# Kernel optimization log

Hardware: AMD Instinct MI355X
Metric: run time of the kernel (lower is better)

The kernel has to match this reference:

```python
import jax, jax.numpy as jnp
import numpy as np

B, T, D, H = 4, 3072, 1024, 16
HD = D // H

def setup_inputs() -> dict:
    key = jax.random.key(0)
    ks = jax.random.split(key, 7)
    s = 1.0 / np.sqrt(D)
    x = jax.random.normal(ks[0], (B, T, D), dtype=jnp.float32)
    Wq = jax.random.normal(ks[1], (D, D), dtype=jnp.float32) * s
    Wk = jax.random.normal(ks[2], (D, D), dtype=jnp.float32) * s
    Wv = jax.random.normal(ks[3], (D, D), dtype=jnp.float32) * s
    Wo = jax.random.normal(ks[4], (D, D), dtype=jnp.float32) * s
    bo = jnp.zeros((D,), dtype=jnp.float32)
    Wconv = jax.random.normal(ks[5], (D, D, 3), dtype=jnp.float32) * (1.0 / np.sqrt(3 * D))  # (out, in, kw)
    return {"x": x, "Wq": Wq, "Wk": Wk, "Wv": Wv, "Wo": Wo, "bo": bo, "Wconv": Wconv}

def reference(x, Wq, Wk, Wv, Wo, bo, Wconv):
    b, t, d = x.shape
    # stride-3 conv pooling of K/V stream (Conv1d(D, D, 3, stride=3, bias=False))
    kc = jax.lax.conv_general_dilated(
        x.transpose(0, 2, 1), Wconv, window_strides=(3,), padding='VALID',
        dimension_numbers=('NCH', 'OIH', 'NCH')).transpose(0, 2, 1)  # (B, T//3, D)
    k_tmp = jnp.concatenate([x[:, :1, :], kc], axis=1)  # (B, Tk, D)
    tk = k_tmp.shape[1]
    # comparison-based bias mask: masked where 3*k_idx >= q_idx + 0.001
    q_idx = jnp.arange(t, dtype=jnp.float32)
    k_idx = jnp.arange(tk, dtype=jnp.float32)
    mask = (k_idx[None, :] * 3.0 >= q_idx[:, None] + 0.001).astype(x.dtype)  # (T, Tk)
    # projections (torch Linear: y = x @ W.T)
    q = x @ Wq.T
    k = k_tmp @ Wk.T
    v = k_tmp @ Wv.T
    q = q.reshape(b, t, H, HD).transpose(0, 2, 1, 3)   # (B, H, T, HD)
    k = k.reshape(b, tk, H, HD).transpose(0, 2, 1, 3)  # (B, H, Tk, HD)
    v = v.reshape(b, tk, H, HD).transpose(0, 2, 1, 3)
    scores = jnp.einsum('bhqd,bhkd->bhqk', q, k) * (HD ** -0.5)
    scores = scores + mask * jnp.asarray(-1e9, dtype=x.dtype)
    p = jax.nn.softmax(scores, axis=-1)  # dropout is identity in eval (p=0)
    o = jnp.einsum('bhqk,bhkd->bhqd', p, v)
    o = o.transpose(0, 2, 1, 3).reshape(b, t, d)
    return o @ Wo.T + bo
```

## Files before the change

### kernel.cpp

```cpp
#include <hip/hip_runtime.h>
#include <hip/hip_bf16.h>
#include <cstdint>
#include <cstddef>

typedef __attribute__((ext_vector_type(8))) __bf16 bf16x8;
typedef __attribute__((ext_vector_type(4))) __bf16 bf16x4;
typedef __attribute__((ext_vector_type(4))) float  floatx4;

#define MFMA16x16x32(a, b, c) __builtin_amdgcn_mfma_f32_16x16x32_bf16((a), (b), (c), 0, 0, 0)

#define ATTN_SC 0.18033688011112042f

__device__ __forceinline__ void gload_lds16(const void* g, void* l) {
  __builtin_amdgcn_global_load_lds((const __attribute__((address_space(1))) void*)g,
                                   (__attribute__((address_space(3))) void*)l,
                                   16, 0, 0);
}


__global__ void prep_kernel(const float* __restrict__ x,
                            const float* __restrict__ Wq, const float* __restrict__ Wk,
                            const float* __restrict__ Wv, const float* __restrict__ Wo,
                            const float* __restrict__ Wconv,
                            __bf16* __restrict__ xb,
                            __bf16* __restrict__ wqb, __bf16* __restrict__ wkb,
                            __bf16* __restrict__ wvb, __bf16* __restrict__ wob,
                            __bf16* __restrict__ wc2, __bf16* __restrict__ ktmp) {
  const int bid = blockIdx.x, tid = threadIdx.x;
  if (bid < 4096) {
    const int which = bid >> 10;
    const float* src = (which == 0) ? Wq : (which == 1) ? Wk : (which == 2) ? Wv : Wo;
    __bf16* dst = (which == 0) ? wqb : (which == 1) ? wkb : (which == 2) ? wvb : wob;
    const int i = (bid & 1023) * 256 + tid;
    floatx4 v = *(const floatx4*)(src + (size_t)i * 4);
    bf16x4 o; o[0] = (__bf16)v[0]; o[1] = (__bf16)v[1]; o[2] = (__bf16)v[2]; o[3] = (__bf16)v[3];
    *(bf16x4*)(dst + (size_t)i * 4) = o;
  } else if (bid < 5120) {
    const int t = (bid - 4096) * 256 + tid;
    const int o = t >> 8, c = t & 255;
    const float* base = Wconv + (size_t)o * 3072 + c * 12;
    float f[12];
    *(floatx4*)(f)     = *(const floatx4*)(base);
    *(floatx4*)(f + 4) = *(const floatx4*)(base + 4);
    *(floatx4*)(f + 8) = *(const floatx4*)(base + 8);
#pragma unroll
    for (int kw = 0; kw < 3; ++kw) {
      bf16x4 q;
#pragma unroll
      for (int j = 0; j < 4; ++j) q[j] = (__bf16)f[3 * j + kw];
      *(bf16x4*)(wc2 + (size_t)o * 3072 + kw * 1024 + c * 4) = q;
    }
  } else if (bid < 5136) {
    const int i = (bid - 5120) * 256 + tid;
    const int b = i >> 10, c = i & 1023;
    ktmp[(size_t)b * 1025 * 1024 + c] = (__bf16)x[(size_t)b * 3072 * 1024 + c];
  } else {
    const int i = (bid - 5136) * 256 + tid;
    floatx4 v = *(const floatx4*)(x + (size_t)i * 4);
    bf16x4 o; o[0] = (__bf16)v[0]; o[1] = (__bf16)v[1]; o[2] = (__bf16)v[2]; o[3] = (__bf16)v[3];
    *(bf16x4*)(xb + (size_t)i * 4) = o;
  }
}

__global__ void vtrans_kernel(const __bf16* __restrict__ V, __bf16* __restrict__ Vt) {
  __shared__ __attribute__((aligned(16))) __bf16 tile[64][72];
  const int tid = threadIdx.x;
  const int bh = blockIdx.y;
  const int b = bh >> 4, h = bh & 15;
  const int t0 = blockIdx.x * 64;
  const int r = tid >> 3, s = tid & 7;
#pragma unroll
  for (int p = 0; p < 2; ++p) {
    const int t = p * 32 + r;
    bf16x8 v = *(const bf16x8*)(V + ((size_t)(b * 1025 + t0 + t)) * 1024 + h * 64 + s * 8);
    *(bf16x8*)(&tile[t][s * 8]) = v;
  }
  __syncthreads();
#pragma unroll
  for (int p = 0; p < 2; ++p) {
    const int d = p * 32 + r;
    bf16x8 o;
#pragma unroll
    for (int e = 0; e < 8; ++e) o[e] = tile[s * 8 + e][d];
    *(bf16x8*)(Vt + ((size_t)bh * 64 + d) * 1024 + t0 + s * 8) = o;
  }
}


template <int MODE>
__device__ __forceinline__ void gemm_body(
    const __bf16* __restrict__ A, const __bf16* __restrict__ Bw, void* __restrict__ Cout,
    const float* __restrict__ bias, int N, int K, int m0, int n0,
    __bf16* As, __bf16* Bs)
{
  const int tid  = threadIdx.x;
  const int wave = tid >> 6;
  const int lane = tid & 63;
  const int g    = lane >> 4;
  const int ln   = lane & 15;
  const int wr = (wave >> 1) * 64;
  const int wc = (wave & 1) * 64;
  const int lr = lane >> 2;
  const int lc = (lane & 3) * 8;

  floatx4 acc[4][4];
#pragma unroll
  for (int i = 0; i < 4; ++i)
#pragma unroll
    for (int j = 0; j < 4; ++j) { floatx4 z = {0.f, 0.f, 0.f, 0.f}; acc[i][j] = z; }

  for (int k0 = 0; k0 < K; k0 += 32) {
    __syncthreads();
#pragma unroll
    for (int i = 0; i < 2; ++i) {
      const int rr = (wave * 2 + i) * 16 + lr;
      gload_lds16(A  + (size_t)(m0 + rr) * K + k0 + lc, As + rr * 32 + lc);
      gload_lds16(Bw + (size_t)(n0 + rr) * K + k0 + lc, Bs + rr * 32 + lc);
    }
    __syncthreads();
    bf16x8 af[4], bfr[4];
#pragma unroll
    for (int i = 0; i < 4; ++i) af[i]  = *(const bf16x8*)(As + (wr + i * 16 + ln) * 32 + g * 8);
#pragma unroll
    for (int j = 0; j < 4; ++j) bfr[j] = *(const bf16x8*)(Bs + (wc + j * 16 + ln) * 32 + g * 8);
#pragma unroll
    for (int i = 0; i < 4; ++i)
#pragma unroll
      for (int j = 0; j < 4; ++j)
        acc[i][j] = MFMA16x16x32(af[i], bfr[j], acc[i][j]);
  }

#pragma unroll
  for (int j = 0; j < 4; ++j) {
    const int col = n0 + wc + j * 16 + ln;
    float bj = 0.f;
    if (MODE == 2) bj = bias[col];
#pragma unroll
    for (int i = 0; i < 4; ++i)
#pragma unroll
      for (int r = 0; r < 4; ++r) {
        const int row = m0 + wr + i * 16 + g * 4 + r;
        if (MODE == 2) {
          ((float*)Cout)[(size_t)row * N + col] = acc[i][j][r] + bj;
        } else if (MODE == 1) {
          const size_t orow = (size_t)(row >> 10) * 1025 + 1 + (row & 1023);
          ((__bf16*)Cout)[orow * 1024 + col] = (__bf16)acc[i][j][r];
        } else if (MODE == 4) {
          ((__bf16*)Cout)[(size_t)row * N + col] = (__bf16)(acc[i][j][r] * ATTN_SC);
        } else {
          ((__bf16*)Cout)[(size_t)row * N + col] = (__bf16)acc[i][j][r];
        }
      }
  }
}

__global__ __launch_bounds__(256) void gemm_convq_kernel(
    const __bf16* __restrict__ xb, const __bf16* __restrict__ wc2,
    const __bf16* __restrict__ wqb, __bf16* __restrict__ ktmp, __bf16* __restrict__ qb)
{
  __shared__ __attribute__((aligned(16))) __bf16 As[128 * 32];
  __shared__ __attribute__((aligned(16))) __bf16 Bs[128 * 32];
  const int bid = blockIdx.x;
  if (bid < 256) {
    gemm_body<1>(xb, wc2, ktmp, nullptr, 1024, 3072, (bid >> 3) * 128, (bid & 7) * 128, As, Bs);
  } else {
    const int t = bid - 256;
    gemm_body<4>(xb, wqb, qb, nullptr, 1024, 1024, (t >> 3) * 128, (t & 7) * 128, As, Bs);
  }
}

__global__ __launch_bounds__(256) void gemm_kv_kernel(
    const __bf16* __restrict__ ktmp, const __bf16* __restrict__ wkb,
    const __bf16* __restrict__ wvb, __bf16* __restrict__ kb, __bf16* __restrict__ vb)
{
  __shared__ __attribute__((aligned(16))) __bf16 As[128 * 32];
  __shared__ __attribute__((aligned(16))) __bf16 Bs[128 * 32];
  const __bf16* Bw = blockIdx.z ? wvb : wkb;
  __bf16* C = blockIdx.z ? vb : kb;
  gemm_body<0>(ktmp, Bw, C, nullptr, 1024, 1024, blockIdx.y * 128, blockIdx.x * 128, As, Bs);
}

__global__ __launch_bounds__(256) void gemm_o_kernel(
    const __bf16* __restrict__ ob, const __bf16* __restrict__ wob,
    float* __restrict__ out, const float* __restrict__ bo)
{
  __shared__ __attribute__((aligned(16))) __bf16 As[128 * 32];
  __shared__ __attribute__((aligned(16))) __bf16 Bs[128 * 32];
  gemm_body<2>(ob, wob, out, bo, 1024, 1024, blockIdx.y * 128, blockIdx.x * 128, As, Bs);
}


__global__ __launch_bounds__(256) void attn_kernel(
    const __bf16* __restrict__ Q, const __bf16* __restrict__ Kk,
    const __bf16* __restrict__ Vt, __bf16* __restrict__ O)
{
  __shared__ __attribute__((aligned(16))) __bf16 Kd[2][64 * 64];
  __shared__ __attribute__((aligned(16))) __bf16 Vd[2][64 * 64];
  __shared__ __attribute__((aligned(16))) __bf16 Ps[4][32 * 64];

  const int tid  = threadIdx.x;
  const int wave = tid >> 6;
  const int lane = tid & 63;
  const int g    = lane >> 4;
  const int ln   = lane & 15;

  const int l    = blockIdx.x;
  const int xcd  = l & 7;
  const int b    = xcd >> 1;
  const int rest = l >> 3;
  const int h    = rest & 15;
  const int qt   = ((11 - (rest >> 4)) << 1) | (xcd & 1);
  const int q0   = qt * 128 + wave * 32;

  const size_t qrow0 = (size_t)b * 3072 + q0;
  const size_t krow0 = (size_t)b * 1025;
  const size_t vtrow = ((size_t)(b * 16 + h)) * 64;
  const int hc = h * 64;
  const int sw = (ln & 7) << 3;
  __bf16* Pw = Ps[wave];

  const int srow = lane >> 3;
  const int scol = (lane & 7) * 8;

  auto stage = [&](int kt, int bb) {
    const int kb0 = kt * 64;
#pragma unroll
    for (int i = 0; i < 2; ++i) {
      const int rr = (wave * 2 + i) * 8 + srow;
      gload_lds16(Kk + (krow0 + kb0 + rr) * 1024 + hc + scol,
                  Kd[bb] + (size_t)rr * 64 + scol);
      gload_lds16(Vt + (vtrow + rr) * 1024 + kb0 + scol,
                  Vd[bb] + (size_t)rr * 64 + scol);
    }
  };

  bf16x8 qf[2][2];
#pragma unroll
  for (int i = 0; i < 2; ++i)
#pragma unroll
    for (int kc = 0; kc < 2; ++kc)
      qf[i][kc] = *(const bf16x8*)(Q + (qrow0 + i * 16 + ln) * 1024 + hc + kc * 32 + g * 8);

  floatx4 oacc[2][4];
  floatx4 oal[2];
#pragma unroll
  for (int i = 0; i < 2; ++i) {
    floatx4 z = {0.f, 0.f, 0.f, 0.f};
    oal[i] = z;
#pragma unroll
    for (int dt = 0; dt < 4; ++dt) oacc[i][dt] = z;
  }

  bf16x8 ones;
#pragma unroll
  for (int e = 0; e < 8; ++e) ones[e] = (__bf16)1.0f;

  const int nkt_blk = (((qt * 128 + 127) / 3) >> 6) + 1;
  const int nfull   = (q0 >= 189) ? ((q0 - 189) / 192 + 1) : 0;

  stage(0, 0);

  for (int kt = 0; kt < nkt_blk; ++kt) {
    const int bb = kt & 1;
    __syncthreads();
    if (kt + 1 < nkt_blk) stage(kt + 1, bb ^ 1);
    const int kb0 = kt * 64;
    const bool masked = (kt >= nfull);

    bf16x8 kf[4][2];
#pragma unroll
    for (int jk = 0; jk < 4; ++jk)
#pragma unroll
      for (int kc = 0; kc < 2; ++kc)
        kf[jk][kc] = *(const bf16x8*)(Kd[bb] + (jk * 16 + ln) * 64 + kc * 32 + g * 8);

#pragma unroll
    for (int jk = 0; jk < 4; ++jk)
#pragma unroll
      for (int i = 0; i < 2; ++i) {
        floatx4 s = {0.f, 0.f, 0.f, 0.f};
        s = MFMA16x16x32(kf[jk][0], qf[i][0], s);
        s = MFMA16x16x32(kf[jk][1], qf[i][1], s);
        float p[4];
#pragma unroll
        for (int r = 0; r < 4; ++r) {
          float e = __builtin_amdgcn_exp2f(s[r]);
          if (masked) {
            const int key = kb0 + jk * 16 + 4 * g + r;
            const int q   = q0 + i * 16 + ln;
            e = (3 * key <= q) ? e : 0.f;
          }
          p[r] = e;
        }
        bf16x4 pk;
        pk[0] = (__bf16)p[0]; pk[1] = (__bf16)p[1]; pk[2] = (__bf16)p[2]; pk[3] = (__bf16)p[3];
        *(bf16x4*)(Pw + (i * 16 + ln) * 64 + ((jk * 16 + 4 * g) ^ sw)) = pk;
      }

#pragma unroll
    for (int kc = 0; kc < 2; ++kc) {
      bf16x8 pf0 = *(const bf16x8*)(Pw + (ln) * 64      + ((kc * 32 + g * 8) ^ sw));
      bf16x8 pf1 = *(const bf16x8*)(Pw + (16 + ln) * 64 + ((kc * 32 + g * 8) ^ sw));
      oal[0] = MFMA16x16x32(ones, pf0, oal[0]);
      oal[1] = MFMA16x16x32(ones, pf1, oal[1]);
#pragma unroll
      for (int dt = 0; dt < 4; ++dt) {
        bf16x8 vf = *(const bf16x8*)(Vd[bb] + (dt * 16 + ln) * 64 + kc * 32 + g * 8);
        oacc[0][dt] = MFMA16x16x32(vf, pf0, oacc[0][dt]);
        oacc[1][dt] = MFMA16x16x32(vf, pf1, oacc[1][dt]);
      }
    }
  }

#pragma unroll
  for (int i = 0; i < 2; ++i) {
    const float inv = 1.0f / oal[i][0];
    const size_t row = qrow0 + i * 16 + ln;
#pragma unroll
    for (int dt = 0; dt < 4; ++dt) {
      bf16x4 o4;
#pragma unroll
      for (int r = 0; r < 4; ++r) o4[r] = (__bf16)(oacc[i][dt][r] * inv);
      *(bf16x4*)(O + row * 1024 + hc + dt * 16 + 4 * g) = o4;
    }
  }
}


extern "C" void kernel_launch(void* const* d_in, const int* in_sizes, int n_in,
                              void* d_out, int out_size, void* d_ws, size_t ws_size,
                              hipStream_t stream) {
  (void)in_sizes; (void)n_in; (void)out_size; (void)ws_size;
  const float* x     = (const float*)d_in[0];
  const float* Wq    = (const float*)d_in[1];
  const float* Wk    = (const float*)d_in[2];
  const float* Wv    = (const float*)d_in[3];
  const float* Wo    = (const float*)d_in[4];
  const float* bo    = (const float*)d_in[5];
  const float* Wconv = (const float*)d_in[6];

  char* ws = (char*)d_ws;
  const size_t SZ_XQ = (size_t)12288 * 1024 * 2;
  const size_t SZ_KT = (size_t)4224 * 1024 * 2;
  const size_t SZ_W  = (size_t)1024 * 1024 * 2;

  __bf16* xb   = (__bf16*)(ws);
  __bf16* qb   = (__bf16*)(ws + SZ_XQ);
  __bf16* ktmp = (__bf16*)(ws + 2 * SZ_XQ);
  __bf16* kb   = (__bf16*)(ws + 2 * SZ_XQ + SZ_KT);
  __bf16* vb   = (__bf16*)(ws + 2 * SZ_XQ + 2 * SZ_KT);
  __bf16* wqb  = (__bf16*)(ws + 2 * SZ_XQ + 3 * SZ_KT);
  __bf16* wkb  = (__bf16*)(ws + 2 * SZ_XQ + 3 * SZ_KT + SZ_W);
  __bf16* wvb  = (__bf16*)(ws + 2 * SZ_XQ + 3 * SZ_KT + 2 * SZ_W);
  __bf16* wob  = (__bf16*)(ws + 2 * SZ_XQ + 3 * SZ_KT + 3 * SZ_W);
  __bf16* wc2  = (__bf16*)(ws + 2 * SZ_XQ + 3 * SZ_KT + 4 * SZ_W);
  __bf16* vt   = xb;

  prep_kernel<<<dim3(17424), dim3(256), 0, stream>>>(x, Wq, Wk, Wv, Wo, Wconv,
                                                     xb, wqb, wkb, wvb, wob, wc2, ktmp);
  gemm_convq_kernel<<<dim3(1024), dim3(256), 0, stream>>>(xb, wc2, wqb, ktmp, qb);
  gemm_kv_kernel<<<dim3(8, 33, 2), dim3(256), 0, stream>>>(ktmp, wkb, wvb, kb, vb);
  vtrans_kernel<<<dim3(16, 64), dim3(256), 0, stream>>>(vb, vt);
  attn_kernel<<<dim3(1536), dim3(256), 0, stream>>>(qb, kb, vt, qb);
  gemm_o_kernel<<<dim3(8, 96, 1), dim3(256), 0, stream>>>(qb, wob, (float*)d_out, bo);
}
```

Measured before the change: 333.3 us.

## Rewrite GEMMs with 128x256 tiles, 4-stage LDS pipeline, swizzle, XCD-aware mapping

Measured after the change: 377.7 us. +13.3%, slower.

```diff
diff --git a/kernel.cpp b/kernel.cpp
--- a/kernel.cpp
+++ b/kernel.cpp
@@ -88,7 +88,7 @@
 
 
 template <int MODE>
-__device__ __forceinline__ void gemm_body(
+__device__ __forceinline__ void gemm8_body(
     const __bf16* __restrict__ A, const __bf16* __restrict__ Bw, void* __restrict__ Cout,
     const float* __restrict__ bias, int N, int K, int m0, int n0,
     __bf16* As, __bf16* Bs)
@@ -98,10 +98,31 @@
   const int lane = tid & 63;
   const int g    = lane >> 4;
   const int ln   = lane & 15;
-  const int wr = (wave >> 1) * 64;
-  const int wc = (wave & 1) * 64;
-  const int lr = lane >> 2;
-  const int lc = (lane & 3) * 8;
+  const int wr   = (wave >> 2) * 64;
+  const int wc   = (wave & 3) * 64;
+
+  const int prow = tid >> 3;
+  const int pc   = tid & 7;
+  const int ca   = pc ^ (prow & 7);
+  const size_t aSrc  = (size_t)(m0 + prow + ((ca >> 2) << 6)) * K + ((ca & 3) << 3);
+  const size_t bSrc0 = (size_t)(n0 + prow + ((ca >> 2) << 7)) * K + ((ca & 3) << 3);
+  const size_t bSrc1 = bSrc0 + (size_t)64 * K;
+
+  int aOff[4], bOff[4];
+#pragma unroll
+  for (int i = 0; i < 4; ++i) {
+    const int ra = wr + i * 16 + ln;
+    const int pr = ra & 63;
+    const int c  = ((ra >> 6) << 2) + g;
+    aOff[i] = pr * 64 + ((c ^ (pr & 7)) << 3);
+  }
+#pragma unroll
+  for (int j = 0; j < 4; ++j) {
+    const int rb = wc + j * 16 + ln;
+    const int pr = rb & 127;
+    const int c  = ((rb >> 7) << 2) + g;
+    bOff[j] = pr * 64 + ((c ^ (pr & 7)) << 3);
+  }
 
   floatx4 acc[4][4];
 #pragma unroll
@@ -109,26 +130,52 @@
 #pragma unroll
     for (int j = 0; j < 4; ++j) { floatx4 z = {0.f, 0.f, 0.f, 0.f}; acc[i][j] = z; }
 
-  for (int k0 = 0; k0 < K; k0 += 32) {
-    __syncthreads();
-#pragma unroll
-    for (int i = 0; i < 2; ++i) {
-      const int rr = (wave * 2 + i) * 16 + lr;
-      gload_lds16(A  + (size_t)(m0 + rr) * K + k0 + lc, As + rr * 32 + lc);
-      gload_lds16(Bw + (size_t)(n0 + rr) * K + k0 + lc, Bs + rr * 32 + lc);
-    }
-    __syncthreads();
-    bf16x8 af[4], bfr[4];
-#pragma unroll
-    for (int i = 0; i < 4; ++i) af[i]  = *(const bf16x8*)(As + (wr + i * 16 + ln) * 32 + g * 8);
-#pragma unroll
-    for (int j = 0; j < 4; ++j) bfr[j] = *(const bf16x8*)(Bs + (wc + j * 16 + ln) * 32 + g * 8);
+  __bf16* const ad0 = As + (tid << 3);
+  __bf16* const bd0 = Bs + (tid << 3);
+
+  auto STAGE = [&](int t, int half) {
+    const int koff = t * 64 + ((half & 1) << 5);
+    gload_lds16(A  + aSrc  + koff, ad0 + (half << 12));
+    gload_lds16(Bw + bSrc0 + koff, bd0 + (half << 13));
+    gload_lds16(Bw + bSrc1 + koff, bd0 + (half << 13) + 4096);
+  };
+
+  auto COMPUTE = [&](int half) {
+    __builtin_amdgcn_sched_barrier(0);
+    const __bf16* ah = As + (half << 12);
+    const __bf16* bh = Bs + (half << 13);
+    bf16x8 af[4], bf[4];
+#pragma unroll
+    for (int i = 0; i < 4; ++i) af[i] = *(const bf16x8*)(ah + aOff[i]);
+#pragma unroll
+    for (int j = 0; j < 4; ++j) bf[j] = *(const bf16x8*)(bh + bOff[j]);
+    asm volatile("s_waitcnt lgkmcnt(0)" ::: "memory");
+    __builtin_amdgcn_sched_barrier(0);
+    __builtin_amdgcn_s_setprio(1);
 #pragma unroll
     for (int i = 0; i < 4; ++i)
 #pragma unroll
       for (int j = 0; j < 4; ++j)
-        acc[i][j] = MFMA16x16x32(af[i], bfr[j], acc[i][j]);
-  }
+        acc[i][j] = MFMA16x16x32(af[i], bf[j], acc[i][j]);
+    __builtin_amdgcn_s_setprio(0);
+  };
+
+  STAGE(0, 0);
+  STAGE(0, 1);
+  const int HT = K >> 5;
+  for (int h = 0; h < HT - 2; ++h) {
+    STAGE((h + 2) >> 1, (h + 2) & 3);
+    asm volatile("s_waitcnt vmcnt(6)" ::: "memory");
+    __builtin_amdgcn_s_barrier();
+    COMPUTE(h & 3);
+    __builtin_amdgcn_s_barrier();
+  }
+  asm volatile("s_waitcnt vmcnt(3)" ::: "memory");
+  __builtin_amdgcn_s_barrier();
+  COMPUTE((HT - 2) & 3);
+  asm volatile("s_waitcnt vmcnt(0)" ::: "memory");
+  __builtin_amdgcn_s_barrier();
+  COMPUTE((HT - 1) & 3);
 
 #pragma unroll
   for (int j = 0; j < 4; ++j) {
@@ -154,39 +201,43 @@
   }
 }
 
-__global__ __launch_bounds__(256) void gemm_convq_kernel(
+__global__ __launch_bounds__(512, 2) void gemm_convq_kernel(
     const __bf16* __restrict__ xb, const __bf16* __restrict__ wc2,
     const __bf16* __restrict__ wqb, __bf16* __restrict__ ktmp, __bf16* __restrict__ qb)
 {
-  __shared__ __attribute__((aligned(16))) __bf16 As[128 * 32];
-  __shared__ __attribute__((aligned(16))) __bf16 Bs[128 * 32];
-  const int bid = blockIdx.x;
-  if (bid < 256) {
-    gemm_body<1>(xb, wc2, ktmp, nullptr, 1024, 3072, (bid >> 3) * 128, (bid & 7) * 128, As, Bs);
+  __shared__ __attribute__((aligned(16))) __bf16 As[16384];
+  __shared__ __attribute__((aligned(16))) __bf16 Bs[32768];
+  const int xcd = blockIdx.x & 7, s = blockIdx.x >> 3;
+  if (s < 16) {
+    const int id = xcd * 16 + s;
+    gemm8_body<1>(xb, wc2, ktmp, nullptr, 1024, 3072, (id >> 2) * 128, (id & 3) * 256, As, Bs);
   } else {
-    const int t = bid - 256;
-    gemm_body<4>(xb, wqb, qb, nullptr, 1024, 1024, (t >> 3) * 128, (t & 7) * 128, As, Bs);
-  }
-}
-
-__global__ __launch_bounds__(256) void gemm_kv_kernel(
+    const int id = xcd * 48 + (s - 16);
+    gemm8_body<4>(xb, wqb, qb, nullptr, 1024, 1024, (id >> 2) * 128, (id & 3) * 256, As, Bs);
+  }
+}
+
+__global__ __launch_bounds__(512, 2) void gemm_kv_kernel(
     const __bf16* __restrict__ ktmp, const __bf16* __restrict__ wkb,
     const __bf16* __restrict__ wvb, __bf16* __restrict__ kb, __bf16* __restrict__ vb)
 {
-  __shared__ __attribute__((aligned(16))) __bf16 As[128 * 32];
-  __shared__ __attribute__((aligned(16))) __bf16 Bs[128 * 32];
-  const __bf16* Bw = blockIdx.z ? wvb : wkb;
-  __bf16* C = blockIdx.z ? vb : kb;
-  gemm_body<0>(ktmp, Bw, C, nullptr, 1024, 1024, blockIdx.y * 128, blockIdx.x * 128, As, Bs);
-}
-
-__global__ __launch_bounds__(256) void gemm_o_kernel(
+  __shared__ __attribute__((aligned(16))) __bf16 As[16384];
+  __shared__ __attribute__((aligned(16))) __bf16 Bs[32768];
+  const int id = (blockIdx.x & 7) * 33 + (blockIdx.x >> 3);
+  const int p  = (id >= 132) ? 1 : 0;
+  const int rest = id - p * 132;
+  gemm8_body<0>(ktmp, p ? wvb : wkb, p ? vb : kb, nullptr, 1024, 1024,
+                (rest >> 2) * 128, (rest & 3) * 256, As, Bs);
+}
+
+__global__ __launch_bounds__(512, 2) void gemm_o_kernel(
     const __bf16* __restrict__ ob, const __bf16* __restrict__ wob,
     float* __restrict__ out, const float* __restrict__ bo)
 {
-  __shared__ __attribute__((aligned(16))) __bf16 As[128 * 32];
-  __shared__ __attribute__((aligned(16))) __bf16 Bs[128 * 32];
-  gemm_body<2>(ob, wob, out, bo, 1024, 1024, blockIdx.y * 128, blockIdx.x * 128, As, Bs);
+  __shared__ __attribute__((aligned(16))) __bf16 As[16384];
+  __shared__ __attribute__((aligned(16))) __bf16 Bs[32768];
+  const int id = (blockIdx.x & 7) * 48 + (blockIdx.x >> 3);
+  gemm8_body<2>(ob, wob, out, bo, 1024, 1024, (id >> 2) * 128, (id & 3) * 256, As, Bs);
 }
 
 
@@ -358,9 +409,9 @@
 
   prep_kernel<<<dim3(17424), dim3(256), 0, stream>>>(x, Wq, Wk, Wv, Wo, Wconv,
                                                      xb, wqb, wkb, wvb, wob, wc2, ktmp);
-  gemm_convq_kernel<<<dim3(1024), dim3(256), 0, stream>>>(xb, wc2, wqb, ktmp, qb);
-  gemm_kv_kernel<<<dim3(8, 33, 2), dim3(256), 0, stream>>>(ktmp, wkb, wvb, kb, vb);
+  gemm_convq_kernel<<<dim3(512), dim3(512), 0, stream>>>(xb, wc2, wqb, ktmp, qb);
+  gemm_kv_kernel<<<dim3(264), dim3(512), 0, stream>>>(ktmp, wkb, wvb, kb, vb);
   vtrans_kernel<<<dim3(16, 64), dim3(256), 0, stream>>>(vb, vt);
   attn_kernel<<<dim3(1536), dim3(256), 0, stream>>>(qb, kb, vt, qb);
-  gemm_o_kernel<<<dim3(8, 96, 1), dim3(256), 0, stream>>>(qb, wob, (float*)d_out, bo);
-}
+  gemm_o_kernel<<<dim3(384), dim3(512), 0, stream>>>(qb, wob, (float*)d_out, bo);
+}
```

## Replace GEMMs with 256x256 double-buffered swizzled tiles and split-K conv with work queue

Applied to the files above, without the earlier changes.

Result: slower. 359.4 us (+7.8%).

```diff
diff --git a/kernel.cpp b/kernel.cpp
--- a/kernel.cpp
+++ b/kernel.cpp
@@ -5,6 +5,7 @@
 
 typedef __attribute__((ext_vector_type(8))) __bf16 bf16x8;
 typedef __attribute__((ext_vector_type(4))) __bf16 bf16x4;
+typedef __attribute__((ext_vector_type(8))) _Float16 halfx8;
 typedef __attribute__((ext_vector_type(4))) float  floatx4;
 
 #define MFMA16x16x32(a, b, c) __builtin_amdgcn_mfma_f32_16x16x32_bf16((a), (b), (c), 0, 0, 0)
@@ -25,8 +26,10 @@
                             __bf16* __restrict__ xb,
                             __bf16* __restrict__ wqb, __bf16* __restrict__ wkb,
                             __bf16* __restrict__ wvb, __bf16* __restrict__ wob,
-                            __bf16* __restrict__ wc2, __bf16* __restrict__ ktmp) {
+                            __bf16* __restrict__ wc2, __bf16* __restrict__ ktmp,
+                            unsigned* __restrict__ cnt) {
   const int bid = blockIdx.x, tid = threadIdx.x;
+  if (bid == 0 && tid == 0) *cnt = 0;
   if (bid < 4096) {
     const int which = bid >> 10;
     const float* src = (which == 0) ? Wq : (which == 1) ? Wk : (which == 2) ? Wv : Wo;
@@ -88,9 +91,9 @@
 
 
 template <int MODE>
-__device__ __forceinline__ void gemm_body(
+__device__ __forceinline__ void gemm256_body(
     const __bf16* __restrict__ A, const __bf16* __restrict__ Bw, void* __restrict__ Cout,
-    const float* __restrict__ bias, int N, int K, int m0, int n0,
+    const float* __restrict__ bias, int lda, int ldb, int m0, int n0, int mMax,
     __bf16* As, __bf16* Bs)
 {
   const int tid  = threadIdx.x;
@@ -98,37 +101,98 @@
   const int lane = tid & 63;
   const int g    = lane >> 4;
   const int ln   = lane & 15;
-  const int wr = (wave >> 1) * 64;
-  const int wc = (wave & 1) * 64;
-  const int lr = lane >> 2;
-  const int lc = (lane & 3) * 8;
-
-  floatx4 acc[4][4];
-#pragma unroll
-  for (int i = 0; i < 4; ++i)
+  const int wr   = (wave >> 2) * 128;
+  const int wc   = (wave & 3) * 64;
+
+  const int prow = tid >> 3;
+  const int ca   = (tid & 7) ^ (prow & 7);
+  const size_t aS = (size_t)(m0 + prow) * lda + ca * 8;
+  const size_t bS = (size_t)(n0 + prow) * ldb + ca * 8;
+  const size_t a64 = (size_t)64 * lda, b64 = (size_t)64 * ldb;
+
+  const int sx0 = ((g ^ (ln & 7)) << 3);
+  const int sx1 = (((4 + g) ^ (ln & 7)) << 3);
+
+  floatx4 acc[8][4];
+#pragma unroll
+  for (int i = 0; i < 8; ++i)
 #pragma unroll
     for (int j = 0; j < 4; ++j) { floatx4 z = {0.f, 0.f, 0.f, 0.f}; acc[i][j] = z; }
 
-  for (int k0 = 0; k0 < K; k0 += 32) {
-    __syncthreads();
-#pragma unroll
-    for (int i = 0; i < 2; ++i) {
-      const int rr = (wave * 2 + i) * 16 + lr;
-      gload_lds16(A  + (size_t)(m0 + rr) * K + k0 + lc, As + rr * 32 + lc);
-      gload_lds16(Bw + (size_t)(n0 + rr) * K + k0 + lc, Bs + rr * 32 + lc);
-    }
-    __syncthreads();
-    bf16x8 af[4], bfr[4];
-#pragma unroll
-    for (int i = 0; i < 4; ++i) af[i]  = *(const bf16x8*)(As + (wr + i * 16 + ln) * 32 + g * 8);
-#pragma unroll
-    for (int j = 0; j < 4; ++j) bfr[j] = *(const bf16x8*)(Bs + (wc + j * 16 + ln) * 32 + g * 8);
-#pragma unroll
-    for (int i = 0; i < 4; ++i)
-#pragma unroll
-      for (int j = 0; j < 4; ++j)
-        acc[i][j] = MFMA16x16x32(af[i], bfr[j], acc[i][j]);
-  }
+  auto STG_A = [&](int t, int buf, int a) {
+    gload_lds16(A + aS + a * a64 + (size_t)t * 64, As + (buf << 14) + (a << 12) + (tid << 3));
+  };
+  auto STG_B = [&](int t, int buf, int a) {
+    gload_lds16(Bw + bS + a * b64 + (size_t)t * 64, Bs + (buf << 14) + (a << 12) + (tid << 3));
+  };
+
+  bf16x8 bfr[4][2];
+  bf16x8 aE[2][2], aO[2][2];
+
+#define RD_B(Bb)                                                                   \
+  { _Pragma("unroll")                                                              \
+    for (int j_ = 0; j_ < 4; ++j_) {                                               \
+      bfr[j_][0] = *(const bf16x8*)((Bb) + (wc + 16 * j_ + ln) * 64 + sx0);        \
+      bfr[j_][1] = *(const bf16x8*)((Bb) + (wc + 16 * j_ + ln) * 64 + sx1);        \
+    } }
+
+#define RD_A(SET, Ab, q)                                                           \
+  { _Pragma("unroll")                                                              \
+    for (int i_ = 0; i_ < 2; ++i_) {                                               \
+      SET[i_][0] = *(const bf16x8*)((Ab) + (wr + 16 * (2 * (q) + i_) + ln) * 64 + sx0); \
+      SET[i_][1] = *(const bf16x8*)((Ab) + (wr + 16 * (2 * (q) + i_) + ln) * 64 + sx1); \
+    } }
+
+#define MF_Q(SET, q)                                                               \
+  { __builtin_amdgcn_s_setprio(1);                                                 \
+    _Pragma("unroll")                                                              \
+    for (int c_ = 0; c_ < 2; ++c_)                                                 \
+      _Pragma("unroll")                                                            \
+      for (int i_ = 0; i_ < 2; ++i_)                                               \
+        _Pragma("unroll")                                                          \
+        for (int j_ = 0; j_ < 4; ++j_)                                             \
+          acc[2 * (q) + i_][j_] = MFMA16x16x32(SET[i_][c_], bfr[j_][c_], acc[2 * (q) + i_][j_]); \
+    __builtin_amdgcn_s_setprio(0); }
+
+  const int NT = 16;
+
+  STG_A(0, 0, 0); STG_A(0, 0, 1); STG_A(0, 0, 2); STG_A(0, 0, 3);
+  STG_B(0, 0, 0); STG_B(0, 0, 1); STG_B(0, 0, 2); STG_B(0, 0, 3);
+  asm volatile("s_waitcnt vmcnt(0)" ::: "memory");
+  __builtin_amdgcn_s_barrier();
+  __builtin_amdgcn_sched_barrier(0);
+  RD_A(aE, As, 0);
+
+  for (int t = 0; t < NT; ++t) {
+    const int buf = t & 1;
+    const __bf16* Ab  = As + (buf << 14);
+    const __bf16* Bb  = Bs + (buf << 14);
+    const __bf16* Abn = As + ((buf ^ 1) << 14);
+    const bool more = (t + 1 < NT);
+    if (more) { STG_A(t + 1, buf ^ 1, 0); STG_A(t + 1, buf ^ 1, 1); STG_B(t + 1, buf ^ 1, 0); }
+    RD_B(Bb);
+    RD_A(aO, Ab, 1);
+    MF_Q(aE, 0);
+    if (more) { STG_A(t + 1, buf ^ 1, 2); STG_A(t + 1, buf ^ 1, 3); STG_B(t + 1, buf ^ 1, 1); }
+    RD_A(aE, Ab, 2);
+    MF_Q(aO, 1);
+    if (more) { STG_B(t + 1, buf ^ 1, 2); STG_B(t + 1, buf ^ 1, 3); }
+    RD_A(aO, Ab, 3);
+    MF_Q(aE, 2);
+    if (more) {
+      asm volatile("s_waitcnt vmcnt(0)" ::: "memory");
+      __builtin_amdgcn_s_barrier();
+      __builtin_amdgcn_sched_barrier(0);
+      RD_A(aE, Abn, 0);
+    }
+    MF_Q(aO, 3);
+    __builtin_amdgcn_s_barrier();
+    __builtin_amdgcn_sched_barrier(0);
+  }
+
+#undef RD_B
+#undef RD_A
+#undef MF_Q
 
 #pragma unroll
   for (int j = 0; j < 4; ++j) {
@@ -136,57 +200,94 @@
     float bj = 0.f;
     if (MODE == 2) bj = bias[col];
 #pragma unroll
-    for (int i = 0; i < 4; ++i)
+    for (int i = 0; i < 8; ++i)
 #pragma unroll
       for (int r = 0; r < 4; ++r) {
         const int row = m0 + wr + i * 16 + g * 4 + r;
         if (MODE == 2) {
-          ((float*)Cout)[(size_t)row * N + col] = acc[i][j][r] + bj;
+          ((float*)Cout)[(size_t)row * 1024 + col] = acc[i][j][r] + bj;
         } else if (MODE == 1) {
           const size_t orow = (size_t)(row >> 10) * 1025 + 1 + (row & 1023);
           ((__bf16*)Cout)[orow * 1024 + col] = (__bf16)acc[i][j][r];
         } else if (MODE == 4) {
-          ((__bf16*)Cout)[(size_t)row * N + col] = (__bf16)(acc[i][j][r] * ATTN_SC);
+          ((__bf16*)Cout)[(size_t)row * 1024 + col] = (__bf16)(acc[i][j][r] * ATTN_SC);
+        } else if (MODE == 5) {
+          ((_Float16*)Cout)[(size_t)row * 1024 + col] = (_Float16)acc[i][j][r];
         } else {
-          ((__bf16*)Cout)[(size_t)row * N + col] = (__bf16)acc[i][j][r];
+          if (row < mMax) ((__bf16*)Cout)[(size_t)row * 1024 + col] = (__bf16)acc[i][j][r];
         }
       }
   }
 }
 
-__global__ __launch_bounds__(256) void gemm_convq_kernel(
+__global__ __launch_bounds__(512, 2) void gemm_convq_kernel(
     const __bf16* __restrict__ xb, const __bf16* __restrict__ wc2,
-    const __bf16* __restrict__ wqb, __bf16* __restrict__ ktmp, __bf16* __restrict__ qb)
+    const __bf16* __restrict__ wqb, __bf16* __restrict__ ktmp, __bf16* __restrict__ qb,
+    _Float16* __restrict__ P0, _Float16* __restrict__ P1, unsigned* __restrict__ cnt)
 {
-  __shared__ __attribute__((aligned(16))) __bf16 As[128 * 32];
-  __shared__ __attribute__((aligned(16))) __bf16 Bs[128 * 32];
-  const int bid = blockIdx.x;
-  if (bid < 256) {
-    gemm_body<1>(xb, wc2, ktmp, nullptr, 1024, 3072, (bid >> 3) * 128, (bid & 7) * 128, As, Bs);
-  } else {
-    const int t = bid - 256;
-    gemm_body<4>(xb, wqb, qb, nullptr, 1024, 1024, (t >> 3) * 128, (t & 7) * 128, As, Bs);
-  }
-}
-
-__global__ __launch_bounds__(256) void gemm_kv_kernel(
+  __shared__ __attribute__((aligned(16))) __bf16 As[32768];
+  __shared__ __attribute__((aligned(16))) __bf16 Bs[32768];
+  __shared__ unsigned widx;
+  for (;;) {
+    if (threadIdx.x == 0) widx = atomicAdd(cnt, 1u);
+    __syncthreads();
+    const unsigned it = widx;
+    __syncthreads();
+    if (it >= 384u) break;
+    if (it < 192u) {
+      const int tap = (int)it >> 6, tile = (int)it & 63;
+      const int m0 = (tile >> 2) * 256, n0 = (tile & 3) * 256;
+      if (tap == 2)
+        gemm256_body<1>(xb + 2048, wc2 + 2048, ktmp, nullptr, 3072, 3072, m0, n0, 1 << 30, As, Bs);
+      else if (tap == 1)
+        gemm256_body<5>(xb + 1024, wc2 + 1024, P1, nullptr, 3072, 3072, m0, n0, 1 << 30, As, Bs);
+      else
+        gemm256_body<5>(xb, wc2, P0, nullptr, 3072, 3072, m0, n0, 1 << 30, As, Bs);
+    } else {
+      const int qid = (int)it - 192;
+      gemm256_body<4>(xb, wqb, qb, nullptr, 1024, 1024, (qid >> 2) * 256, (qid & 3) * 256,
+                      1 << 30, As, Bs);
+    }
+  }
+}
+
+__global__ void reduce_conv_kernel(const _Float16* __restrict__ P0, const _Float16* __restrict__ P1,
+                                   __bf16* __restrict__ ktmp) {
+  const int idx = blockIdx.x * 256 + threadIdx.x;
+  const int r = idx >> 7;
+  const int c = (idx & 127) * 8;
+  const size_t orow = (size_t)(r >> 10) * 1025 + 1 + (r & 1023);
+  __bf16* kp = ktmp + orow * 1024 + c;
+  bf16x8 k8 = *(const bf16x8*)kp;
+  halfx8 p0 = *(const halfx8*)(P0 + (size_t)r * 1024 + c);
+  halfx8 p1 = *(const halfx8*)(P1 + (size_t)r * 1024 + c);
+  bf16x8 o;
+#pragma unroll
+  for (int e = 0; e < 8; ++e) o[e] = (__bf16)((float)k8[e] + (float)p0[e] + (float)p1[e]);
+  *(bf16x8*)kp = o;
+}
+
+__global__ __launch_bounds__(512, 2) void gemm_kv_kernel(
     const __bf16* __restrict__ ktmp, const __bf16* __restrict__ wkb,
     const __bf16* __restrict__ wvb, __bf16* __restrict__ kb, __bf16* __restrict__ vb)
 {
-  __shared__ __attribute__((aligned(16))) __bf16 As[128 * 32];
-  __shared__ __attribute__((aligned(16))) __bf16 Bs[128 * 32];
-  const __bf16* Bw = blockIdx.z ? wvb : wkb;
-  __bf16* C = blockIdx.z ? vb : kb;
-  gemm_body<0>(ktmp, Bw, C, nullptr, 1024, 1024, blockIdx.y * 128, blockIdx.x * 128, As, Bs);
-}
-
-__global__ __launch_bounds__(256) void gemm_o_kernel(
+  __shared__ __attribute__((aligned(16))) __bf16 As[32768];
+  __shared__ __attribute__((aligned(16))) __bf16 Bs[32768];
+  const int id = (blockIdx.x & 7) * 17 + (blockIdx.x >> 3);
+  const int p  = (id >= 68) ? 1 : 0;
+  const int rest = id - p * 68;
+  gemm256_body<0>(ktmp, p ? wvb : wkb, p ? vb : kb, nullptr, 1024, 1024,
+                  (rest >> 2) * 256, (rest & 3) * 256, 4100, As, Bs);
+}
+
+__global__ __launch_bounds__(512, 2) void gemm_o_kernel(
     const __bf16* __restrict__ ob, const __bf16* __restrict__ wob,
     float* __restrict__ out, const float* __restrict__ bo)
 {
-  __shared__ __attribute__((aligned(16))) __bf16 As[128 * 32];
-  __shared__ __attribute__((aligned(16))) __bf16 Bs[128 * 32];
-  gemm_body<2>(ob, wob, out, bo, 1024, 1024, blockIdx.y * 128, blockIdx.x * 128, As, Bs);
+  __shared__ __attribute__((aligned(16))) __bf16 As[32768];
+  __shared__ __attribute__((aligned(16))) __bf16 Bs[32768];
+  const int id = (blockIdx.x & 7) * 24 + (blockIdx.x >> 3);
+  gemm256_body<2>(ob, wob, out, bo, 1024, 1024, (id >> 2) * 256, (id & 3) * 256, 1 << 30, As, Bs);
 }
 
 
@@ -356,11 +457,16 @@
   __bf16* wc2  = (__bf16*)(ws + 2 * SZ_XQ + 3 * SZ_KT + 4 * SZ_W);
   __bf16* vt   = xb;
 
+  _Float16* P0 = (_Float16*)kb;
+  _Float16* P1 = (_Float16*)vb;
+  unsigned* cnt = (unsigned*)((char*)ktmp + 8396800);
+
   prep_kernel<<<dim3(17424), dim3(256), 0, stream>>>(x, Wq, Wk, Wv, Wo, Wconv,
-                                                     xb, wqb, wkb, wvb, wob, wc2, ktmp);
-  gemm_convq_kernel<<<dim3(1024), dim3(256), 0, stream>>>(xb, wc2, wqb, ktmp, qb);
-  gemm_kv_kernel<<<dim3(8, 33, 2), dim3(256), 0, stream>>>(ktmp, wkb, wvb, kb, vb);
+                                                     xb, wqb, wkb, wvb, wob, wc2, ktmp, cnt);
+  gemm_convq_kernel<<<dim3(256), dim3(512), 0, stream>>>(xb, wc2, wqb, ktmp, qb, P0, P1, cnt);
+  reduce_conv_kernel<<<dim3(2048), dim3(256), 0, stream>>>(P0, P1, ktmp);
+  gemm_kv_kernel<<<dim3(136), dim3(512), 0, stream>>>(ktmp, wkb, wvb, kb, vb);
   vtrans_kernel<<<dim3(16, 64), dim3(256), 0, stream>>>(vb, vt);
   attn_kernel<<<dim3(1536), dim3(256), 0, stream>>>(qb, kb, vt, qb);
-  gemm_o_kernel<<<dim3(8, 96, 1), dim3(256), 0, stream>>>(qb, wob, (float*)d_out, bo);
-}
+  gemm_o_kernel<<<dim3(192), dim3(512), 0, stream>>>(qb, wob, (float*)d_out, bo);
+}
```
